# Kernel tuning notes

Hardware: AMD Instinct MI355X
Metric: run time of the kernel (lower is better)

## Reference

```python
import jax, jax.numpy as jnp
import numpy as np

GX, GY, NH = 480, 360, 32
EPS = 1e-5


def _bn(x, g, b):
    # torch BatchNorm1d training-mode stats over the point dimension
    m = jnp.mean(x, axis=0)
    v = jnp.mean((x - m) ** 2, axis=0)
    return g * (x - m) / jnp.sqrt(v + EPS) + b


def setup_inputs():
    key = jax.random.key(0)
    ks = jax.random.split(key, 24)
    B, N, F = 2, 120000, 7
    s = 0.02
    inp = {
        "pt_fea": jax.random.normal(ks[0], (B, N, F), jnp.float32),
        "xy_ind": jax.random.randint(ks[1], (B, N, 2), 0, 360, dtype=jnp.int32),
        "bn0_g": jnp.ones((7,), jnp.float32), "bn0_b": jnp.zeros((7,), jnp.float32),
        "W1": jax.random.normal(ks[2], (7, 64), jnp.float32) * s,  "b1": jnp.zeros((64,), jnp.float32),
        "bn1_g": jnp.ones((64,), jnp.float32), "bn1_b": jnp.zeros((64,), jnp.float32),
        "W2": jax.random.normal(ks[3], (64, 128), jnp.float32) * s, "b2": jnp.zeros((128,), jnp.float32),
        "bn2_g": jnp.ones((128,), jnp.float32), "bn2_b": jnp.zeros((128,), jnp.float32),
        "W3": jax.random.normal(ks[4], (128, 256), jnp.float32) * s, "b3": jnp.zeros((256,), jnp.float32),
        "bn3_g": jnp.ones((256,), jnp.float32), "bn3_b": jnp.zeros((256,), jnp.float32),
        "W4": jax.random.normal(ks[5], (256, 512), jnp.float32) * s, "b4": jnp.zeros((512,), jnp.float32),
        "W5": jax.random.normal(ks[6], (512, NH), jnp.float32) * s, "b5": jnp.zeros((NH,), jnp.float32),
    }
    return inp


def _forward_sample(fea, xy, bn0_g, bn0_b, W1, b1, bn1_g, bn1_b, W2, b2,
                    bn2_g, bn2_b, W3, b3, bn3_g, bn3_b, W4, b4, W5, b5):
    # Simplified PointNet: BN -> (Linear, BN, ReLU) x3 -> Linear
    x = _bn(fea, bn0_g, bn0_b)
    x = jax.nn.relu(_bn(x @ W1 + b1, bn1_g, bn1_b))
    x = jax.nn.relu(_bn(x @ W2 + b2, bn2_g, bn2_b))
    x = jax.nn.relu(_bn(x @ W3 + b3, bn3_g, bn3_b))
    x = x @ W4 + b4                              # [N, 512]
    # per-voxel segment max over flattened BEV cell id
    ids = xy[:, 0] * GY + xy[:, 1]               # [N]
    nseg = GX * GY
    seg = jax.ops.segment_max(x, ids, num_segments=nseg)   # [nseg, 512]
    cnt = jax.ops.segment_sum(jnp.ones(ids.shape[0], x.dtype), ids, num_segments=nseg)
    occ = (cnt > 0)[:, None]
    seg = jnp.where(occ, seg, 0.0)               # empty voxels -> 0 (scatter semantics)
    nh = jax.nn.relu(seg @ W5 + b5)              # fea_compression
    nh = jnp.where(occ, nh, 0.0)
    return nh.reshape(GX, GY, NH).transpose(2, 0, 1)  # [NH, GX, GY]


def reference(pt_fea, xy_ind, bn0_g, bn0_b, W1, b1, bn1_g, bn1_b, W2, b2,
              bn2_g, bn2_b, W3, b3, bn3_g, bn3_b, W4, b4, W5, b5):
    f = lambda fea, xy: _forward_sample(fea, xy, bn0_g, bn0_b, W1, b1, bn1_g, bn1_b,
                                        W2, b2, bn2_g, bn2_b, W3, b3, bn3_g, bn3_b,
                                        W4, b4, W5, b5)
    return jax.vmap(f)(pt_fea, xy_ind)           # [B, NH, GX, GY]
```

## Files before the change

kernel.cpp:

```cpp
#include <hip/hip_runtime.h>
#include <cstdint>

#define GXD 480
#define GYD 360
#define NHD 32
#define NPTS 120000
#define MPAD 120064
#define MB128 (MPAD/128)
#define SEGR 129600
#define NSEG (GXD*GYD)
#define EPSB 1e-5f

using short8 = __attribute__((ext_vector_type(8))) short;
using f32x4  = __attribute__((ext_vector_type(4))) float;

__device__ __forceinline__ float bf2f(unsigned short u) {
    return __uint_as_float(((unsigned int)u) << 16);
}
__device__ __forceinline__ unsigned short f2bf(float f) {
    unsigned int u = __float_as_uint(f);
    u += 0x7fffu + ((u >> 16) & 1u);
    return (unsigned short)(u >> 16);
}
__device__ __forceinline__ unsigned int bnrelu_pack(unsigned int wv, float sc0, float sh0,
                                                    float sc1, float sh1)
{
    float lo = __uint_as_float(wv << 16);
    float hi = __uint_as_float(wv & 0xffff0000u);
    lo = fmaxf(fmaf(lo, sc0, sh0), 0.f);
    hi = fmaxf(fmaf(hi, sc1, sh1), 0.f);
    unsigned int r;
    asm("v_cvt_pk_bf16_f32 %0, %1, %2" : "=v"(r) : "v"(lo), "v"(hi));
    return r;
}
__device__ __forceinline__ unsigned int pk_bf16(float lo, float hi)
{
    unsigned int r;
    asm("v_cvt_pk_bf16_f32 %0, %1, %2" : "=v"(r) : "v"(lo), "v"(hi));
    return r;
}

__device__ __forceinline__ void async16(const unsigned short* g, unsigned short* l)
{
    __builtin_amdgcn_global_load_lds(
        (const __attribute__((address_space(1))) unsigned int*)g,
        (__attribute__((address_space(3))) unsigned int*)l, 16, 0, 0);
}

__global__ __launch_bounds__(256) void bn0_stats_kernel(
    const float* __restrict__ fea, float* __restrict__ s0, float* __restrict__ q0)
{
    float s[7] = {0,0,0,0,0,0,0}, q[7] = {0,0,0,0,0,0,0};
    for (int p = blockIdx.x * 256 + threadIdx.x; p < NPTS; p += gridDim.x * 256) {
        const float* r = fea + (size_t)p * 7;
#pragma unroll
        for (int f = 0; f < 7; ++f) { float v = r[f]; s[f] += v; q[f] += v * v; }
    }
    __shared__ float red[256];
    int t = threadIdx.x;
#pragma unroll
    for (int f = 0; f < 7; ++f) {
        red[t] = s[f]; __syncthreads();
        for (int o = 128; o > 0; o >>= 1) {
            if (t < o) red[t] += red[t + o];
            __syncthreads();
        }
        if (t == 0) atomicAdd(&s0[f], red[0]);
        __syncthreads();
        red[t] = q[f]; __syncthreads();
        for (int o = 128; o > 0; o >>= 1) {
            if (t < o) red[t] += red[t + o];
            __syncthreads();
        }
        if (t == 0) atomicAdd(&q0[f], red[0]);
        __syncthreads();
    }
}

__global__ void prep0_kernel(const float* __restrict__ s0, const float* __restrict__ q0,
                             const float* __restrict__ g0, const float* __restrict__ b0,
                             const float* __restrict__ W1, const float* __restrict__ b1,
                             float* __restrict__ W1p, float* __restrict__ b1p)
{
    __shared__ float sc[7], sh[7];
    int t = threadIdx.x;
    if (t < 7) {
        float m = s0[t] / (float)NPTS;
        float v = q0[t] / (float)NPTS - m * m;
        float inv = 1.0f / sqrtf(fmaxf(v, 0.f) + EPSB);
        sc[t] = g0[t] * inv;
        sh[t] = b0[t] - m * g0[t] * inv;
    }
    __syncthreads();
    if (t < 64) {
        float acc = b1[t];
#pragma unroll
        for (int f = 0; f < 7; ++f) {
            W1p[f * 64 + t] = W1[f * 64 + t] * sc[f];
            acc += sh[f] * W1[f * 64 + t];
        }
        b1p[t] = acc;
    }
}

__global__ void prep_bn_kernel(const float* __restrict__ sum, const float* __restrict__ sq,
                               const float* __restrict__ g, const float* __restrict__ b,
                               float* __restrict__ sc, float* __restrict__ sh, int C)
{
    int c = blockIdx.x * blockDim.x + threadIdx.x;
    if (c < C) {
        float m = sum[c] / (float)NPTS;
        float v = sq[c] / (float)NPTS - m * m;
        float inv = 1.0f / sqrtf(fmaxf(v, 0.f) + EPSB);
        sc[c] = g[c] * inv;
        sh[c] = b[c] - m * g[c] * inv;
    }
}

template<int C>
__global__ __launch_bounds__(256) void bnrelu_kernel(
    unsigned short* __restrict__ Y,
    const float* __restrict__ sc, const float* __restrict__ sh)
{
    __shared__ float scs[C], shs[C];
    int t = threadIdx.x;
    for (int i = t; i < C; i += 256) { scs[i] = sc[i]; shs[i] = sh[i]; }
    __syncthreads();
    const size_t total8 = (size_t)MPAD * C / 8;
    for (size_t i = (size_t)blockIdx.x * 256 + t; i < total8; i += (size_t)gridDim.x * 256) {
        int c0 = (int)((i * 8) & (size_t)(C - 1));
        uint4 v = *(const uint4*)(Y + i * 8);
        float4 s0 = *(const float4*)&scs[c0];
        float4 s1 = *(const float4*)&scs[c0 + 4];
        float4 h0 = *(const float4*)&shs[c0];
        float4 h1 = *(const float4*)&shs[c0 + 4];
        uint4 o;
        o.x = bnrelu_pack(v.x, s0.x, h0.x, s0.y, h0.y);
        o.y = bnrelu_pack(v.y, s0.z, h0.z, s0.w, h0.w);
        o.z = bnrelu_pack(v.z, s1.x, h1.x, s1.y, h1.y);
        o.w = bnrelu_pack(v.w, s1.z, h1.z, s1.w, h1.w);
        *(uint4*)(Y + i * 8) = o;
    }
}

__global__ __launch_bounds__(256) void wtrans_kernel(const float* __restrict__ W,
                                                     unsigned short* __restrict__ Wt,
                                                     int K, int N)
{
    int i = blockIdx.x * 256 + threadIdx.x;
    if (i < K * N) {
        int k = i / N, n = i % N;
        Wt[(size_t)n * K + k] = f2bf(W[i]);
    }
}

__global__ __launch_bounds__(256) void layer1_kernel(
    const float* __restrict__ fea, const float* __restrict__ W1p, const float* __restrict__ b1p,
    unsigned short* __restrict__ y1, float* __restrict__ sum1, float* __restrict__ sq1)
{
    __shared__ float Wl[448], bl[64];
    __shared__ float feaL[256 * 7];
    __shared__ float colsum[64], colsq[64];
    int t = threadIdx.x;
    int p0 = blockIdx.x * 256;
    for (int i = t; i < 448; i += 256) Wl[i] = W1p[i];
    if (t < 64) { bl[t] = b1p[t]; colsum[t] = 0.f; colsq[t] = 0.f; }
    int nval7 = (NPTS - p0) * 7;
    for (int i = t; i < 256 * 7; i += 256)
        feaL[i] = (i < nval7) ? fea[(size_t)p0 * 7 + i] : 0.f;
    __syncthreads();
    int cg = t & 7, pt = t >> 3;
    float s[8] = {}, q[8] = {};
#pragma unroll
    for (int it = 0; it < 8; ++it) {
        int row = it * 32 + pt;
        bool valid = (p0 + row) < NPTS;
        float f[7];
#pragma unroll
        for (int ff = 0; ff < 7; ++ff) f[ff] = feaL[row * 7 + ff];
        float vj[8];
#pragma unroll
        for (int j = 0; j < 8; ++j) {
            int c = cg * 8 + j;
            float v = bl[c];
#pragma unroll
            for (int ff = 0; ff < 7; ++ff) v = fmaf(f[ff], Wl[ff * 64 + c], v);
            vj[j] = v;
            if (valid) { s[j] += v; q[j] += v * v; }
        }
        uint4 ow;
        ow.x = (unsigned int)f2bf(vj[0]) | ((unsigned int)f2bf(vj[1]) << 16);
        ow.y = (unsigned int)f2bf(vj[2]) | ((unsigned int)f2bf(vj[3]) << 16);
        ow.z = (unsigned int)f2bf(vj[4]) | ((unsigned int)f2bf(vj[5]) << 16);
        ow.w = (unsigned int)f2bf(vj[6]) | ((unsigned int)f2bf(vj[7]) << 16);
        *(uint4*)(y1 + (size_t)(p0 + row) * 64 + cg * 8) = ow;
    }
#pragma unroll
    for (int off = 8; off < 64; off <<= 1) {
#pragma unroll
        for (int j = 0; j < 8; ++j) {
            s[j] += __shfl_xor(s[j], off);
            q[j] += __shfl_xor(q[j], off);
        }
    }
    if ((t & 63) < 8) {
#pragma unroll
        for (int j = 0; j < 8; ++j) {
            atomicAdd(&colsum[cg * 8 + j], s[j]);
            atomicAdd(&colsq[cg * 8 + j], q[j]);
        }
    }
    __syncthreads();
    if (t < 64) {
        atomicAdd(&sum1[t], colsum[t]);
        atomicAdd(&sq1[t], colsq[t]);
    }
}

template<int K, int NC, bool STATS>
__global__ __launch_bounds__(256) void gemm_quad(
    const unsigned short* __restrict__ A, const unsigned short* __restrict__ Wt,
    const float* __restrict__ bias, unsigned short* __restrict__ Y,
    float* __restrict__ osum, float* __restrict__ osq)
{
    __shared__ __align__(16) unsigned short lds[16384];
    __shared__ float colsum[128], colsq[128];
    int t = threadIdx.x;
    int w = t >> 6, ln = t & 63, quad = ln >> 4, lr = ln & 15;
    int wr = w >> 1, wc = w & 1;
    const int mbase = blockIdx.y * 128;
    const int cbase = blockIdx.x * 128;
    unsigned short* Asl = lds;
    unsigned short* Bsl = lds + 8192;

    if (STATS && t < 128) { colsum[t] = 0.f; colsq[t] = 0.f; }
    __syncthreads();

    const int srow = w * 16 + (ln >> 2);
    const int koff = (ln & 3) * 8;

    auto stage = [&](int buf, int kt) {
#pragma unroll
        for (int half = 0; half < 2; ++half) {
            int row = half * 64 + srow;
            async16(A  + (size_t)(mbase + row) * K + kt + koff,
                    Asl + buf * 4096 + half * 2048 + w * 512 + ln * 8);
            async16(Wt + (size_t)(cbase + row) * K + kt + koff,
                    Bsl + buf * 4096 + half * 2048 + w * 512 + ln * 8);
        }
    };

    f32x4 acc[4][4];
#pragma unroll
    for (int i = 0; i < 4; ++i)
#pragma unroll
        for (int j = 0; j < 4; ++j) acc[i][j] = (f32x4){0.f, 0.f, 0.f, 0.f};

    stage(0, 0);
    stage(1, 32);

    constexpr int NR = K / 32;
#pragma unroll
    for (int r = 0; r < NR; ++r) {
        const int buf = r & 1;
        if (r + 1 < NR)
            asm volatile("s_waitcnt vmcnt(4)" ::: "memory");
        else
            asm volatile("s_waitcnt vmcnt(0)" ::: "memory");
        asm volatile("s_barrier" ::: "memory");
        short8 af[4], bfr[4];
#pragma unroll
        for (int mi = 0; mi < 4; ++mi)
            af[mi] = *(const short8*)&Asl[buf * 4096 + (wr * 64 + mi * 16 + lr) * 32 + quad * 8];
#pragma unroll
        for (int ni = 0; ni < 4; ++ni)
            bfr[ni] = *(const short8*)&Bsl[buf * 4096 + (wc * 64 + ni * 16 + lr) * 32 + quad * 8];
        asm volatile("s_waitcnt lgkmcnt(0)" ::: "memory");
        asm volatile("s_barrier" ::: "memory");
        if (r + 2 < NR)
            stage(buf, (r + 2) * 32);
#pragma unroll
        for (int mi = 0; mi < 4; ++mi)
#pragma unroll
            for (int ni = 0; ni < 4; ++ni)
                acc[mi][ni] = __builtin_amdgcn_mfma_f32_16x16x32_bf16(
                    af[mi], bfr[ni], acc[mi][ni], 0, 0, 0);
    }
    __syncthreads();

    unsigned short* Cw = lds + w * 4096;
#pragma unroll
    for (int ni = 0; ni < 4; ++ni) {
        int col = ni * 16 + lr;
        float bv = bias[cbase + wc * 64 + col];
        float s = 0.f, q = 0.f;
#pragma unroll
        for (int mi = 0; mi < 4; ++mi) {
            int rb = mi * 16 + quad * 4;
#pragma unroll
            for (int r = 0; r < 4; ++r) {
                float v = acc[mi][ni][r] + bv;
                Cw[(rb + r) * 64 + col] = f2bf(v);
                if (STATS && (mbase + wr * 64 + rb + r) < NPTS) { s += v; q += v * v; }
            }
        }
        if (STATS) {
            atomicAdd(&colsum[wc * 64 + col], s);
            atomicAdd(&colsq[wc * 64 + col], q);
        }
    }
#pragma unroll
    for (int i = 0; i < 8; ++i) {
        int idx = i * 64 + ln;
        int row = idx >> 3, colq = (idx & 7) * 8;
        *(uint4*)(Y + (size_t)(mbase + wr * 64 + row) * NC + cbase + wc * 64 + colq) =
            *(const uint4*)&Cw[row * 64 + colq];
    }
    if (STATS) {
        __syncthreads();
        if (t < 128) {
            atomicAdd(&osum[blockIdx.x * 128 + t], colsum[t]);
            atomicAdd(&osq[blockIdx.x * 128 + t], colsq[t]);
        }
    }
}

__global__ __launch_bounds__(256) void hist_kernel(const int* __restrict__ xy,
                                                   int* __restrict__ cnt)
{
    int p = blockIdx.x * 256 + threadIdx.x;
    if (p < NPTS) {
        int id = xy[(size_t)p * 2] * GYD + xy[(size_t)p * 2 + 1];
        atomicAdd(&cnt[id], 1);
    }
}

__global__ __launch_bounds__(256) void scanA_kernel(const int* __restrict__ cnt,
                                                    int* __restrict__ csum)
{
    __shared__ int red[256];
    int t = threadIdx.x, base = blockIdx.x * 2048;
    int s = 0;
    for (int i = t; i < 2048; i += 256) {
        int idx = base + i;
        if (idx < SEGR) s += cnt[idx];
    }
    red[t] = s; __syncthreads();
    for (int o = 128; o > 0; o >>= 1) { if (t < o) red[t] += red[t + o]; __syncthreads(); }
    if (t == 0) csum[blockIdx.x] = red[0];
}

__global__ void scanB_kernel(int* __restrict__ csum, int* __restrict__ offs)
{
    if (threadIdx.x == 0) {
        int run = 0;
        for (int i = 0; i < 64; ++i) { int v = csum[i]; csum[i] = run; run += v; }
        offs[SEGR] = run;
    }
}

__global__ __launch_bounds__(256) void scanC_kernel(const int* __restrict__ cnt,
                                                    const int* __restrict__ csum,
                                                    int* __restrict__ offs,
                                                    int* __restrict__ cursor)
{
    __shared__ int red[256];
    int t = threadIdx.x, base = blockIdx.x * 2048;
    int v[8]; int s = 0;
#pragma unroll
    for (int i = 0; i < 8; ++i) {
        int idx = base + t * 8 + i;
        v[i] = (idx < SEGR) ? cnt[idx] : 0;
        s += v[i];
    }
    red[t] = s; __syncthreads();
    for (int o = 1; o < 256; o <<= 1) {
        int x = (t >= o) ? red[t - o] : 0;
        __syncthreads();
        red[t] += x;
        __syncthreads();
    }
    int run = red[t] - s + csum[blockIdx.x];
#pragma unroll
    for (int i = 0; i < 8; ++i) {
        int idx = base + t * 8 + i;
        if (idx < SEGR) { offs[idx] = run; cursor[idx] = run; }
        run += v[i];
    }
}

__global__ __launch_bounds__(256) void scatter_idx_kernel(const int* __restrict__ xy,
                                                          int* __restrict__ cursor,
                                                          int* __restrict__ order)
{
    int p = blockIdx.x * 256 + threadIdx.x;
    if (p < NPTS) {
        int id = xy[(size_t)p * 2] * GYD + xy[(size_t)p * 2 + 1];
        int pos = atomicAdd(&cursor[id], 1);
        order[pos] = p;
    }
}

__global__ __launch_bounds__(256) void l4seg_kernel(
    const unsigned short* __restrict__ y3, const unsigned short* __restrict__ Wt4,
    const float* __restrict__ b4, const unsigned short* __restrict__ Wt5,
    const float* __restrict__ b5, const int* __restrict__ offs,
    const int* __restrict__ ord, float* __restrict__ out)
{
    __shared__ __align__(16) unsigned short Bsl[64 * 256];
    __shared__ __align__(16) unsigned short w5s[32 * 64];
    __shared__ __align__(16) unsigned short y4s[64 * 72];
    __shared__ float b4s[512];
    __shared__ int offs_s[65];
    __shared__ int osl[128];
    int t = threadIdx.x;
    int w = t >> 6, ln = t & 63, quad = ln >> 4, lr = ln & 15;
    int c0 = blockIdx.x * 64;
    if (t < 65) offs_s[t] = offs[c0 + t];
    for (int i = t; i < 512; i += 256) b4s[i] = b4[i];
    __syncthreads();
    const int jb = offs_s[0], je = offs_s[64];
    if (jb == je) {
#pragma unroll
        for (int j = 0; j < 8; ++j)
            out[(size_t)(w * 8 + j) * NSEG + c0 + ln] = 0.f;
        return;
    }
    if (t < 128) { int aj = jb + t; osl[t] = (aj < je) ? ord[aj] : 0; }
    __syncthreads();

    const int cell = t >> 2, q = t & 3;
    const int cjb = offs_s[cell], cje = offs_s[cell + 1];

    f32x4 eacc[2];
    eacc[0] = (f32x4){0.f, 0.f, 0.f, 0.f};
    eacc[1] = (f32x4){0.f, 0.f, 0.f, 0.f};

    for (int p = 0; p < 8; ++p) {
#pragma unroll
        for (int i = 0; i < 8; ++i) {
            int rl = w * 16 + i * 2 + (ln >> 5);
            int cl = (ln & 31) ^ (rl & 7);
            async16(Wt4 + (size_t)(p * 64 + rl) * 256 + cl * 8,
                    Bsl + (w * 16 + i * 2) * 256 + ln * 8);
        }
        {
            int rl = t >> 3, cl = (t & 7) ^ (rl & 7);
            async16(Wt5 + (size_t)rl * 512 + p * 64 + cl * 8, w5s + t * 8);
        }
        float mxv[16];
#pragma unroll
        for (int i = 0; i < 16; ++i) mxv[i] = -3.0e38f;

        int chunk = 0;
        for (int cs = jb; cs < je; cs += 64, ++chunk) {
            int j = cs + w * 16 + lr; if (j >= je) j = je - 1;
            int idx = j - jb;
            int pr = (idx < 128) ? osl[idx] : ord[j];
            const unsigned short* Ar = y3 + (size_t)pr * 256 + quad * 8;
            short8 af[8];
#pragma unroll
            for (int r = 0; r < 8; ++r)
                af[r] = *(const short8*)(Ar + r * 32);
            f32x4 acc[4];
#pragma unroll
            for (int i = 0; i < 4; ++i) acc[i] = (f32x4){0.f, 0.f, 0.f, 0.f};
            if (chunk == 0) {
                asm volatile("s_waitcnt vmcnt(0)" ::: "memory");
                asm volatile("s_barrier" ::: "memory");
            }
#pragma unroll
            for (int r = 0; r < 8; ++r) {
                const int cp = (r * 4 + quad) ^ (lr & 7);
#pragma unroll
                for (int ni = 0; ni < 4; ++ni) {
                    short8 bfr = *(const short8*)&Bsl[(ni * 16 + lr) * 256 + cp * 8];
                    acc[ni] = __builtin_amdgcn_mfma_f32_16x16x32_bf16(af[r], bfr, acc[ni], 0, 0, 0);
                }
            }
#pragma unroll
            for (int ni = 0; ni < 4; ++ni) {
                float bv = b4s[p * 64 + ni * 16 + lr];
#pragma unroll
                for (int rr = 0; rr < 4; ++rr)
                    y4s[(w * 16 + quad * 4 + rr) * 72 + ni * 16 + lr] = f2bf(acc[ni][rr] + bv);
            }
            asm volatile("s_waitcnt lgkmcnt(0)" ::: "memory");
            asm volatile("s_barrier" ::: "memory");
            int lo = cjb > cs ? cjb : cs;
            int hi = cje < cs + 64 ? cje : cs + 64;
            for (int jj = lo; jj < hi; ++jj) {
                const uint4* rp = (const uint4*)&y4s[(jj - cs) * 72 + q * 16];
                uint4 v0 = rp[0], v1 = rp[1];
                unsigned int wv[8] = {v0.x, v0.y, v0.z, v0.w, v1.x, v1.y, v1.z, v1.w};
#pragma unroll
                for (int k2 = 0; k2 < 8; ++k2) {
                    mxv[2 * k2]     = fmaxf(mxv[2 * k2],     bf2f((unsigned short)(wv[k2] & 0xffffu)));
                    mxv[2 * k2 + 1] = fmaxf(mxv[2 * k2 + 1], bf2f((unsigned short)(wv[k2] >> 16)));
                }
            }
            asm volatile("s_barrier" ::: "memory");
        }
        {
            bool empty = (cjb == cje);
#pragma unroll
            for (int i = 0; i < 8; ++i) {
                float lo2 = empty ? 0.f : mxv[2 * i], hi2 = empty ? 0.f : mxv[2 * i + 1];
                *(unsigned int*)&y4s[cell * 72 + q * 16 + 2 * i] = pk_bf16(lo2, hi2);
            }
        }
        asm volatile("s_waitcnt lgkmcnt(0)" ::: "memory");
        asm volatile("s_barrier" ::: "memory");
#pragma unroll
        for (int kt = 0; kt < 2; ++kt) {
            short8 af2 = *(const short8*)&y4s[(w * 16 + lr) * 72 + kt * 32 + quad * 8];
            const int cp = (kt * 4 + quad) ^ (lr & 7);
#pragma unroll
            for (int ni = 0; ni < 2; ++ni) {
                short8 bfr = *(const short8*)&w5s[(ni * 16 + lr) * 64 + cp * 8];
                eacc[ni] = __builtin_amdgcn_mfma_f32_16x16x32_bf16(af2, bfr, eacc[ni], 0, 0, 0);
            }
        }
        asm volatile("s_waitcnt lgkmcnt(0)" ::: "memory");
        asm volatile("s_barrier" ::: "memory");
    }
    float* outs = (float*)&Bsl[0];
#pragma unroll
    for (int ni = 0; ni < 2; ++ni) {
        int h = ni * 16 + lr;
        float bv = b5[h];
#pragma unroll
        for (int rr = 0; rr < 4; ++rr) {
            int cr = w * 16 + quad * 4 + rr;
            bool oc = offs_s[cr + 1] > offs_s[cr];
            outs[cr * 33 + h] = oc ? fmaxf(eacc[ni][rr] + bv, 0.f) : 0.f;
        }
    }
    __syncthreads();
#pragma unroll
    for (int j = 0; j < 8; ++j)
        out[(size_t)(w * 8 + j) * NSEG + c0 + ln] = outs[ln * 33 + w * 8 + j];
}

__global__ __launch_bounds__(256) void ztail_kernel(float* __restrict__ out)
{
    int i = blockIdx.x * 256 + threadIdx.x;
    const int per = (NSEG - SEGR) / 4;
    int h = i / per, c = i % per;
    *(float4*)(out + (size_t)h * NSEG + SEGR + (size_t)c * 4) = make_float4(0.f, 0.f, 0.f, 0.f);
}

extern "C" void kernel_launch(void* const* d_in, const int* in_sizes, int n_in,
                              void* d_out, int out_size, void* d_ws, size_t ws_size,
                              hipStream_t stream)
{
    const float* pt_fea = (const float*)d_in[0];
    const int*   xy_ind = (const int*)d_in[1];
    const float* bn0_g  = (const float*)d_in[2];
    const float* bn0_b  = (const float*)d_in[3];
    const float* W1     = (const float*)d_in[4];
    const float* b1     = (const float*)d_in[5];
    const float* bn1_g  = (const float*)d_in[6];
    const float* bn1_b  = (const float*)d_in[7];
    const float* W2     = (const float*)d_in[8];
    const float* b2     = (const float*)d_in[9];
    const float* bn2_g  = (const float*)d_in[10];
    const float* bn2_b  = (const float*)d_in[11];
    const float* W3     = (const float*)d_in[12];
    const float* b3     = (const float*)d_in[13];
    const float* bn3_g  = (const float*)d_in[14];
    const float* bn3_b  = (const float*)d_in[15];
    const float* W4     = (const float*)d_in[16];
    const float* b4     = (const float*)d_in[17];
    const float* W5     = (const float*)d_in[18];
    const float* b5     = (const float*)d_in[19];
    float* out = (float*)d_out;

    const size_t oY2   = 61472768;
    const size_t oE    = oY2 + (size_t)MPAD * 128 * 2;
    const size_t oCnt  = oE + (size_t)SEGR * 32 * 4;
    const size_t oOffs = oCnt + 518400;
    const size_t oCur  = oOffs + 518528;
    const size_t oOrd  = oCur + 518400;
    const size_t oCsum = oOrd + 480000;
    const size_t oSt   = oCsum + 512;
    const size_t oWt2  = oSt + 16384;
    const size_t oWt3  = oWt2 + 16384;
    const size_t oWt4  = oWt3 + 65536;
    const size_t oWt5  = oWt4 + 262144;

    unsigned short* y1   = (unsigned short*)d_ws;
    unsigned short* y3   = (unsigned short*)d_ws;
    unsigned short* y2   = (unsigned short*)((char*)d_ws + oY2);
    int*            cnt  = (int*)((char*)d_ws + oCnt);
    int*            offs = (int*)((char*)d_ws + oOffs);
    int*            cur  = (int*)((char*)d_ws + oCur);
    int*            ord  = (int*)((char*)d_ws + oOrd);
    int*            csum = (int*)((char*)d_ws + oCsum);
    float*          st   = (float*)((char*)d_ws + oSt);
    unsigned short* Wt2  = (unsigned short*)((char*)d_ws + oWt2);
    unsigned short* Wt3  = (unsigned short*)((char*)d_ws + oWt3);
    unsigned short* Wt4  = (unsigned short*)((char*)d_ws + oWt4);
    unsigned short* Wt5  = (unsigned short*)((char*)d_ws + oWt5);

    float* s0 = st + 0;     float* q0 = st + 8;
    float* W1p = st + 16;   float* b1p = st + 464;
    float* sum1 = st + 528; float* sq1 = st + 592; float* sc1 = st + 656; float* sh1 = st + 720;
    float* sum2 = st + 784; float* sq2 = st + 912; float* sc2 = st + 1040; float* sh2 = st + 1168;
    float* sum3 = st + 1296; float* sq3 = st + 1552; float* sc3 = st + 1808; float* sh3 = st + 2064;

    wtrans_kernel<<<(64 * 128 + 255) / 256, 256, 0, stream>>>(W2, Wt2, 64, 128);
    wtrans_kernel<<<(128 * 256 + 255) / 256, 256, 0, stream>>>(W3, Wt3, 128, 256);
    wtrans_kernel<<<(256 * 512 + 255) / 256, 256, 0, stream>>>(W4, Wt4, 256, 512);
    wtrans_kernel<<<(512 * 32 + 255) / 256, 256, 0, stream>>>(W5, Wt5, 512, 32);

    for (int b = 0; b < 2; ++b) {
        const float* fea_b = pt_fea + (size_t)b * NPTS * 7;
        const int*   xy_b  = xy_ind + (size_t)b * NPTS * 2;
        float*       out_b = out + (size_t)b * NHD * NSEG;

        (void)hipMemsetAsync(st, 0, 2320 * sizeof(float), stream);
        (void)hipMemsetAsync(cnt, 0, (size_t)SEGR * 4, stream);

        bn0_stats_kernel<<<128, 256, 0, stream>>>(fea_b, s0, q0);
        prep0_kernel<<<1, 64, 0, stream>>>(s0, q0, bn0_g, bn0_b, W1, b1, W1p, b1p);
        layer1_kernel<<<MPAD / 256, 256, 0, stream>>>(fea_b, W1p, b1p, y1, sum1, sq1);
        prep_bn_kernel<<<1, 64, 0, stream>>>(sum1, sq1, bn1_g, bn1_b, sc1, sh1, 64);
        bnrelu_kernel<64><<<1024, 256, 0, stream>>>(y1, sc1, sh1);
        gemm_quad<64, 128, true><<<dim3(1, MB128), 256, 0, stream>>>(
            y1, Wt2, b2, y2, sum2, sq2);
        prep_bn_kernel<<<1, 128, 0, stream>>>(sum2, sq2, bn2_g, bn2_b, sc2, sh2, 128);
        bnrelu_kernel<128><<<2048, 256, 0, stream>>>(y2, sc2, sh2);
        gemm_quad<128, 256, true><<<dim3(2, MB128), 256, 0, stream>>>(
            y2, Wt3, b3, y3, sum3, sq3);
        prep_bn_kernel<<<1, 256, 0, stream>>>(sum3, sq3, bn3_g, bn3_b, sc3, sh3, 256);
        bnrelu_kernel<256><<<2048, 256, 0, stream>>>(y3, sc3, sh3);

        hist_kernel<<<(NPTS + 255) / 256, 256, 0, stream>>>(xy_b, cnt);
        scanA_kernel<<<64, 256, 0, stream>>>(cnt, csum);
        scanB_kernel<<<1, 64, 0, stream>>>(csum, offs);
        scanC_kernel<<<64, 256, 0, stream>>>(cnt, csum, offs, cur);
        scatter_idx_kernel<<<(NPTS + 255) / 256, 256, 0, stream>>>(xy_b, cur, ord);

        l4seg_kernel<<<SEGR / 64, 256, 0, stream>>>(y3, Wt4, b4, Wt5, b5, offs, ord, out_b);
        ztail_kernel<<<1350, 256, 0, stream>>>(out_b);
    }
}
```

Baseline: 783.1 us.

## Hoist point-row A fragments into registers and prefetch next W4/W5 slice

Loads the first two 64-point chunks of y3 rows into registers once, before the 8-pass loop over output column slices. Before, every pass re-gathered them from global memory. The next pass's W4 and W5 tiles are issued asynchronously as soon as the current slice's MFMA is done, which overlaps the weight fetch with the max-reduction and the W5 MFMA. This costs many more vector registers (two 8x short8 arrays held across the loop), which may lower occupancy. It also depends on barrier ordering to keep Bsl and w5s from being overwritten while still in use.

```diff
diff --git a/kernel.cpp b/kernel.cpp
--- a/kernel.cpp
+++ b/kernel.cpp
@@ -431,12 +431,25 @@
 
     const int cell = t >> 2, q = t & 3;
     const int cjb = offs_s[cell], cje = offs_s[cell + 1];
+    const int nch = (je - jb + 63) >> 6;
+
+    short8 af0[8], af1[8];
+    {
+        int j0 = w * 16 + lr; if (jb + j0 >= je) j0 = je - 1 - jb;
+        const unsigned short* Ar0 = y3 + (size_t)osl[j0] * 256 + quad * 8;
+#pragma unroll
+        for (int r = 0; r < 8; ++r) af0[r] = *(const short8*)(Ar0 + r * 32);
+        int j1 = 64 + w * 16 + lr; if (jb + j1 >= je) j1 = je - 1 - jb;
+        const unsigned short* Ar1 = y3 + (size_t)osl[j1] * 256 + quad * 8;
+#pragma unroll
+        for (int r = 0; r < 8; ++r) af1[r] = *(const short8*)(Ar1 + r * 32);
+    }
 
     f32x4 eacc[2];
     eacc[0] = (f32x4){0.f, 0.f, 0.f, 0.f};
     eacc[1] = (f32x4){0.f, 0.f, 0.f, 0.f};
 
-    for (int p = 0; p < 8; ++p) {
+    auto stageB = [&](int p) {
 #pragma unroll
         for (int i = 0; i < 8; ++i) {
             int rl = w * 16 + i * 2 + (ln >> 5);
@@ -444,38 +457,53 @@
             async16(Wt4 + (size_t)(p * 64 + rl) * 256 + cl * 8,
                     Bsl + (w * 16 + i * 2) * 256 + ln * 8);
         }
-        {
-            int rl = t >> 3, cl = (t & 7) ^ (rl & 7);
-            async16(Wt5 + (size_t)rl * 512 + p * 64 + cl * 8, w5s + t * 8);
-        }
+    };
+    auto stageW5 = [&](int p) {
+        int rl = t >> 3, cl = (t & 7) ^ (rl & 7);
+        async16(Wt5 + (size_t)rl * 512 + p * 64 + cl * 8, w5s + t * 8);
+    };
+    auto mfma_chunk = [&](const short8* af, f32x4* acc) {
+#pragma unroll
+        for (int r = 0; r < 8; ++r) {
+            const int cp = (r * 4 + quad) ^ (lr & 7);
+#pragma unroll
+            for (int ni = 0; ni < 4; ++ni) {
+                short8 bfr = *(const short8*)&Bsl[(ni * 16 + lr) * 256 + cp * 8];
+                acc[ni] = __builtin_amdgcn_mfma_f32_16x16x32_bf16(af[r], bfr, acc[ni], 0, 0, 0);
+            }
+        }
+    };
+
+    stageB(0); stageW5(0);
+
+    for (int p = 0; p < 8; ++p) {
+        asm volatile("s_waitcnt vmcnt(0)" ::: "memory");
+        asm volatile("s_barrier" ::: "memory");
         float mxv[16];
 #pragma unroll
         for (int i = 0; i < 16; ++i) mxv[i] = -3.0e38f;
 
-        int chunk = 0;
-        for (int cs = jb; cs < je; cs += 64, ++chunk) {
-            int j = cs + w * 16 + lr; if (j >= je) j = je - 1;
-            int idx = j - jb;
-            int pr = (idx < 128) ? osl[idx] : ord[j];
-            const unsigned short* Ar = y3 + (size_t)pr * 256 + quad * 8;
-            short8 af[8];
-#pragma unroll
-            for (int r = 0; r < 8; ++r)
-                af[r] = *(const short8*)(Ar + r * 32);
+        for (int c = 0; c < nch; ++c) {
+            const int cs = jb + c * 64;
             f32x4 acc[4];
 #pragma unroll
             for (int i = 0; i < 4; ++i) acc[i] = (f32x4){0.f, 0.f, 0.f, 0.f};
-            if (chunk == 0) {
-                asm volatile("s_waitcnt vmcnt(0)" ::: "memory");
-                asm volatile("s_barrier" ::: "memory");
-            }
-#pragma unroll
-            for (int r = 0; r < 8; ++r) {
-                const int cp = (r * 4 + quad) ^ (lr & 7);
-#pragma unroll
-                for (int ni = 0; ni < 4; ++ni) {
-                    short8 bfr = *(const short8*)&Bsl[(ni * 16 + lr) * 256 + cp * 8];
-                    acc[ni] = __builtin_amdgcn_mfma_f32_16x16x32_bf16(af[r], bfr, acc[ni], 0, 0, 0);
+            if (c == 0) {
+                mfma_chunk(af0, acc);
+            } else if (c == 1) {
+                mfma_chunk(af1, acc);
+            } else {
+                int j = cs + w * 16 + lr; if (j >= je) j = je - 1;
+                const unsigned short* Ar = y3 + (size_t)ord[j] * 256 + quad * 8;
+#pragma unroll
+                for (int r = 0; r < 8; ++r) {
+                    short8 a = *(const short8*)(Ar + r * 32);
+                    const int cp = (r * 4 + quad) ^ (lr & 7);
+#pragma unroll
+                    for (int ni = 0; ni < 4; ++ni) {
+                        short8 bfr = *(const short8*)&Bsl[(ni * 16 + lr) * 256 + cp * 8];
+                        acc[ni] = __builtin_amdgcn_mfma_f32_16x16x32_bf16(a, bfr, acc[ni], 0, 0, 0);
+                    }
                 }
             }
 #pragma unroll
@@ -487,6 +515,8 @@
             }
             asm volatile("s_waitcnt lgkmcnt(0)" ::: "memory");
             asm volatile("s_barrier" ::: "memory");
+            if (c == nch - 1 && p < 7)
+                stageB(p + 1);
             int lo = cjb > cs ? cjb : cs;
             int hi = cje < cs + 64 ? cje : cs + 64;
             for (int jj = lo; jj < hi; ++jj) {
@@ -523,6 +553,7 @@
         }
         asm volatile("s_waitcnt lgkmcnt(0)" ::: "memory");
         asm volatile("s_barrier" ::: "memory");
+        if (p < 7) stageW5(p + 1);
     }
     float* outs = (float*)&Bsl[0];
 #pragma unroll
```

Measured after the change: 787.6 us. About the same (+0.6%).
